# Kernel tuning notes

Hardware: AMD Instinct MI355X
Metric: run time of the kernel (lower is better)

## Reference

```python
import jax, jax.numpy as jnp
import numpy as np

D_MODEL = 1024
N_HEAD = 16
STRIDE = 16
HEAD_DIM = D_MODEL // N_HEAD
B, TQ, TK = 4, 2048, 8192
L = TK // STRIDE  # per-head key count (same for all heads since n_head <= stride and TK % stride == 0)


def setup_inputs() -> dict:
    key = jax.random.key(0)
    ks = jax.random.split(key, 12)
    w_scale = 0.02
    return {
        "q": jax.random.normal(ks[0], (B, TQ, D_MODEL), dtype=jnp.float32),
        "k": jax.random.normal(ks[1], (B, TK, D_MODEL), dtype=jnp.float32),
        "v": jax.random.normal(ks[2], (B, TK, D_MODEL), dtype=jnp.float32),
        "src_mask": jnp.ones((B, 1, 1, TK), dtype=jnp.int32),
        "w_q": jax.random.normal(ks[3], (D_MODEL, D_MODEL), dtype=jnp.float32) * w_scale,
        "b_q": jnp.zeros((D_MODEL,), dtype=jnp.float32),
        "w_k": jax.random.normal(ks[4], (D_MODEL, D_MODEL), dtype=jnp.float32) * w_scale,
        "b_k": jnp.zeros((D_MODEL,), dtype=jnp.float32),
        "w_v": jax.random.normal(ks[5], (D_MODEL, D_MODEL), dtype=jnp.float32) * w_scale,
        "b_v": jnp.zeros((D_MODEL,), dtype=jnp.float32),
        "w_o": jax.random.normal(ks[6], (D_MODEL, D_MODEL), dtype=jnp.float32) * w_scale,
        "b_o": jnp.zeros((D_MODEL,), dtype=jnp.float32),
    }


def reference(q, k, v, src_mask, w_q, b_q, w_k, b_k, w_v, b_v, w_o, b_o):
    # projections (torch Linear: x @ W.T + b)
    Q = (q @ w_q.T + b_q).reshape(B, TQ, N_HEAD, HEAD_DIM).transpose(0, 2, 1, 3)  # [B,H,Tq,D]
    K = (k @ w_k.T + b_k).reshape(B, TK, N_HEAD, HEAD_DIM).transpose(0, 2, 1, 3)  # [B,H,Tk,D]
    V = (v @ w_v.T + b_v).reshape(B, TK, N_HEAD, HEAD_DIM).transpose(0, 2, 1, 3)

    # HEPOS strided per-head key indices: head h attends to positions h, h+stride, ...
    idx = jnp.arange(N_HEAD)[:, None] + STRIDE * jnp.arange(L)[None, :]  # [H,L]
    gidx = idx[None, :, :, None]  # broadcastable over batch and head_dim
    Kh = jnp.take_along_axis(K, gidx, axis=2)  # [B,H,L,D]
    Vh = jnp.take_along_axis(V, gidx, axis=2)  # [B,H,L,D]

    scores = jnp.einsum("bhqd,bhld->bhql", Q, Kh) / jnp.sqrt(jnp.float32(HEAD_DIM))
    # gather per-head mask slice: src_mask [B,1,1,Tk] -> [B,H,1,L]
    mask_b = jnp.broadcast_to(src_mask, (B, N_HEAD, 1, TK))
    mask_h = jnp.take_along_axis(mask_b, idx[None, :, None, :], axis=3)  # [B,H,1,L]
    scores = jnp.where(mask_h == 0, jnp.float32(-1e9), scores)

    attn = jax.nn.softmax(scores, axis=-1)  # dropout is identity in eval mode
    out = jnp.einsum("bhql,bhld->bhqd", attn, Vh)  # [B,H,Tq,D]
    out = out.transpose(0, 2, 1, 3).reshape(B, TQ, D_MODEL)
    return out @ w_o.T + b_o
```

## Files before the change

### kernel.cpp

```cpp
#include <hip/hip_runtime.h>
#include <stdint.h>

#define NBATCH 4
#define TQ 2048
#define TKK 8192
#define DM 1024
#define HDIM 64
#define LLEN 512

typedef __bf16 bf16;
typedef __attribute__((ext_vector_type(4))) float f32x4;
typedef __attribute__((ext_vector_type(8))) __bf16 bf16x8;
typedef __attribute__((ext_vector_type(4))) __bf16 bf16x4;

typedef const __attribute__((address_space(1))) void* gas1_t;
typedef __attribute__((address_space(3))) void* las3_t;

__device__ __forceinline__ void gload_lds16(const void* g, void* l) {
  __builtin_amdgcn_global_load_lds((gas1_t)(uintptr_t)g, (las3_t)(uint32_t)(uintptr_t)l, 16, 0, 0);
}

__device__ __forceinline__ void cast4(const float* __restrict__ src, bf16* __restrict__ dst, int i) {
  float4 v = ((const float4*)src)[i];
  bf16x4 o;
  o[0] = (bf16)v.x; o[1] = (bf16)v.y; o[2] = (bf16)v.z; o[3] = (bf16)v.w;
  ((bf16x4*)dst)[i] = o;
}

__global__ void prep_kernel(const float* __restrict__ q,
                            const float* __restrict__ wq, const float* __restrict__ wk,
                            const float* __restrict__ wv, const float* __restrict__ wo,
                            const int* __restrict__ sm,
                            bf16* __restrict__ QB, bf16* __restrict__ WQ, bf16* __restrict__ WK,
                            bf16* __restrict__ WV, bf16* __restrict__ WO, float* __restrict__ MF) {
  int tid = blockIdx.x * blockDim.x + threadIdx.x;
  int stride = gridDim.x * blockDim.x;
  for (int i = tid; i < 2097152; i += stride) cast4(q, QB, i);
  for (int i = tid; i < 262144; i += stride) cast4(wq, WQ, i);
  for (int i = tid; i < 262144; i += stride) cast4(wk, WK, i);
  for (int i = tid; i < 262144; i += stride) cast4(wv, WV, i);
  for (int i = tid; i < 262144; i += stride) cast4(wo, WO, i);
  for (int i = tid; i < 32768; i += stride) {
    int bh = i >> 9, l = i & 511;
    int b = bh >> 4, h = bh & 15;
    MF[i] = sm[b * TKK + h + 16 * l] ? 1.0f : 0.0f;
  }
}

template<bool OUT_BF16>
__global__ __launch_bounds__(256) void gemm_bt_bias(
    const bf16* __restrict__ A, const bf16* __restrict__ Bm,
    const float* __restrict__ bias, void* __restrict__ Cout, float scale) {
  __shared__ bf16 As[128 * 64];
  __shared__ bf16 Bs[128 * 64];
  const int t = threadIdx.x;
  const int lane = t & 63, w = t >> 6;
  const int wm = w >> 1, wn = w & 1;
  const int bid = blockIdx.x;
  const int swz = (bid & 7) * 64 + (bid >> 3);
  const int m0 = (swz >> 3) * 128, n0 = (swz & 7) * 128;
  const int c = lane & 15, g = lane >> 4;
  f32x4 acc[4][4] = {};
  for (int k0 = 0; k0 < DM; k0 += 64) {
    __syncthreads();
    #pragma unroll
    for (int i = 0; i < 4; ++i) {
      int chunk = i * 256 + t;
      int row = chunk >> 3, blk = chunk & 7;
      gload_lds16(A + (size_t)(m0 + row) * DM + k0 + blk * 8, As + chunk * 8);
      gload_lds16(Bm + (size_t)(n0 + row) * DM + k0 + blk * 8, Bs + chunk * 8);
    }
    __syncthreads();
    #pragma unroll
    for (int kk = 0; kk < 2; ++kk) {
      bf16x8 af[4], bfr[4];
      #pragma unroll
      for (int f = 0; f < 4; ++f)
        af[f] = *(const bf16x8*)(As + (wm * 64 + f * 16 + c) * 64 + kk * 32 + g * 8);
      #pragma unroll
      for (int f = 0; f < 4; ++f)
        bfr[f] = *(const bf16x8*)(Bs + (wn * 64 + f * 16 + c) * 64 + kk * 32 + g * 8);
      #pragma unroll
      for (int mi = 0; mi < 4; ++mi)
        #pragma unroll
        for (int ni = 0; ni < 4; ++ni)
          acc[mi][ni] = __builtin_amdgcn_mfma_f32_16x16x32_bf16(af[mi], bfr[ni], acc[mi][ni], 0, 0, 0);
    }
  }
  #pragma unroll
  for (int ni = 0; ni < 4; ++ni) {
    int n = n0 + wn * 64 + ni * 16 + c;
    float bv = bias[n];
    #pragma unroll
    for (int mi = 0; mi < 4; ++mi) {
      int m = m0 + wm * 64 + mi * 16 + g * 4;
      #pragma unroll
      for (int j = 0; j < 4; ++j) {
        float vv = (acc[mi][ni][j] + bv) * scale;
        if (OUT_BF16) ((bf16*)Cout)[(size_t)(m + j) * DM + n] = (bf16)vv;
        else          ((float*)Cout)[(size_t)(m + j) * DM + n] = vv;
      }
    }
  }
}

__global__ __launch_bounds__(256) void kv_proj_fused(
    const float* __restrict__ Xk, const float* __restrict__ Xv,
    const bf16* __restrict__ WK, const bf16* __restrict__ WV,
    const float* __restrict__ bk, const float* __restrict__ bv,
    bf16* __restrict__ KH, bf16* __restrict__ VTT) {
  __shared__ bf16 As[64 * 64];
  __shared__ bf16 Bs[64 * 64];
  const int t = threadIdx.x, lane = t & 63, w = t >> 6;
  const int wm = w >> 1, wn = w & 1;
  const int bid = blockIdx.x;
  const int swz = (bid & 7) * 128 + (bid >> 3);
  const int iz = swz >> 9;
  const int bh = (swz >> 3) & 63;
  const int ltile = swz & 7;
  const int b = bh >> 4, h = bh & 15;
  const int l0 = ltile * 64;
  const float* __restrict__ X = iz ? Xv : Xk;
  const bf16* __restrict__ W = iz ? WV : WK;
  const float* __restrict__ bias = iz ? bv : bk;
  const int c = lane & 15, g = lane >> 4;
  f32x4 acc[2][2] = {};
  for (int k0 = 0; k0 < DM; k0 += 64) {
    __syncthreads();
    #pragma unroll
    for (int i = 0; i < 4; ++i) {
      int chunk = i * 256 + t;
      int row = chunk >> 4, q4 = chunk & 15;
      float4 vv = *(const float4*)(X + ((size_t)b * TKK + h + 16 * (l0 + row)) * DM + k0 + q4 * 4);
      bf16x4 o;
      o[0] = (bf16)vv.x; o[1] = (bf16)vv.y; o[2] = (bf16)vv.z; o[3] = (bf16)vv.w;
      uint32_t byte = (uint32_t)(row * 128 + q4 * 8) ^ (uint32_t)((row & 7) << 4);
      *(bf16x4*)((char*)As + byte) = o;
    }
    #pragma unroll
    for (int i = 0; i < 2; ++i) {
      int chunk = i * 256 + t;
      int row = chunk >> 3, blk = chunk & 7;
      uint4 vv = *(const uint4*)(W + (size_t)(h * 64 + row) * DM + k0 + blk * 8);
      uint32_t byte = (uint32_t)(row * 128 + blk * 16) ^ (uint32_t)((row & 7) << 4);
      *(uint4*)((char*)Bs + byte) = vv;
    }
    __syncthreads();
    #pragma unroll
    for (int kk = 0; kk < 2; ++kk) {
      bf16x8 af[2], bfr[2];
      #pragma unroll
      for (int f = 0; f < 2; ++f) {
        int row = wm * 32 + f * 16 + c;
        uint32_t byte = (uint32_t)(row * 128 + (kk * 32 + g * 8) * 2) ^ (uint32_t)((row & 7) << 4);
        af[f] = *(const bf16x8*)((char*)As + byte);
      }
      #pragma unroll
      for (int f = 0; f < 2; ++f) {
        int row = wn * 32 + f * 16 + c;
        uint32_t byte = (uint32_t)(row * 128 + (kk * 32 + g * 8) * 2) ^ (uint32_t)((row & 7) << 4);
        bfr[f] = *(const bf16x8*)((char*)Bs + byte);
      }
      #pragma unroll
      for (int mi = 0; mi < 2; ++mi)
        #pragma unroll
        for (int ni = 0; ni < 2; ++ni)
          acc[mi][ni] = __builtin_amdgcn_mfma_f32_16x16x32_bf16(af[mi], bfr[ni], acc[mi][ni], 0, 0, 0);
    }
  }
  #pragma unroll
  for (int ni = 0; ni < 2; ++ni) {
    int n = wn * 32 + ni * 16 + c;
    float bvv = bias[h * 64 + n];
    #pragma unroll
    for (int mi = 0; mi < 2; ++mi) {
      int m = wm * 32 + mi * 16 + g * 4;
      if (iz == 0) {
        #pragma unroll
        for (int j = 0; j < 4; ++j)
          KH[((size_t)bh * LLEN + l0 + m + j) * 64 + n] = (bf16)(acc[mi][ni][j] + bvv);
      } else {
        bf16x4 o;
        #pragma unroll
        for (int j = 0; j < 4; ++j) o[j] = (bf16)(acc[mi][ni][j] + bvv);
        *(bf16x4*)(VTT + ((size_t)bh * 64 + n) * LLEN + l0 + m) = o;
      }
    }
  }
}

__device__ __forceinline__ void stage_kv(const bf16* __restrict__ KH, const bf16* __restrict__ VT,
                                         bf16* Ks, bf16* Vs, int bh, int lt, int t) {
  #pragma unroll
  for (int i = 0; i < 4; ++i) {
    int chunk = i * 256 + t, row = chunk >> 3, blk = chunk & 7;
    uint4 v = *(const uint4*)(KH + ((size_t)bh * LLEN + lt * 128 + row) * 64 + blk * 8);
    uint32_t byte = (uint32_t)(row * 128 + blk * 16) ^ (uint32_t)((row & 7) << 4);
    *(uint4*)((char*)Ks + byte) = v;
  }
  #pragma unroll
  for (int i = 0; i < 4; ++i) {
    int chunk = i * 256 + t, row = chunk >> 4, blk = chunk & 15;
    uint4 v = *(const uint4*)(VT + ((size_t)bh * 64 + row) * LLEN + lt * 128 + blk * 8);
    uint32_t byte = (uint32_t)(row * 256 + blk * 16) ^ (uint32_t)((row & 7) << 4);
    *(uint4*)((char*)Vs + byte) = v;
  }
}

__global__ __launch_bounds__(256) void attn_kernel(
    const bf16* __restrict__ Qp, const bf16* __restrict__ KH, const bf16* __restrict__ VT,
    const float* __restrict__ maskf, bf16* __restrict__ AO) {
  __shared__ bf16 Qs[128 * 64];
  __shared__ bf16 Ks[128 * 64];
  __shared__ bf16 Vs[64 * 128];
  const int t = threadIdx.x, lane = t & 63, w = t >> 6;
  const int bid = blockIdx.x;
  const int swz = (bid & 7) * 128 + (bid >> 3);
  const int bh = swz >> 4, b = bh >> 4, h = bh & 15;
  const int q0 = (swz & 15) * 128;
  const int c = lane & 15, g = lane >> 4;

  #pragma unroll
  for (int i = 0; i < 4; ++i) {
    int chunk = i * 256 + t, row = chunk >> 3, blk = chunk & 7;
    uint4 v = *(const uint4*)(Qp + ((size_t)(b * TQ + q0 + row)) * DM + h * 64 + blk * 8);
    uint32_t byte = (uint32_t)(row * 128 + blk * 16) ^ (uint32_t)((row & 7) << 4);
    *(uint4*)((char*)Qs + byte) = v;
  }
  stage_kv(KH, VT, Ks, Vs, bh, 0, t);
  __syncthreads();

  bf16x8 bq[2][2];
  #pragma unroll
  for (int nf = 0; nf < 2; ++nf)
    #pragma unroll
    for (int kk = 0; kk < 2; ++kk) {
      int row = w * 32 + nf * 16 + c;
      uint32_t byte = (uint32_t)(row * 128 + (kk * 32 + g * 8) * 2) ^ (uint32_t)((row & 7) << 4);
      bq[nf][kk] = *(const bf16x8*)((char*)Qs + byte);
    }

  float m_run[2] = {-1e30f, -1e30f};
  float l_run[2] = {0.0f, 0.0f};
  f32x4 acc_o[4][2] = {};

  #pragma unroll 1
  for (int lt = 0; lt < 4; ++lt) {
    f32x4 s[8][2] = {};
    #pragma unroll
    for (int kk = 0; kk < 2; ++kk) {
      bf16x8 ak[8];
      #pragma unroll
      for (int mf = 0; mf < 8; ++mf) {
        int row = mf * 16 + c;
        uint32_t byte = (uint32_t)(row * 128 + (kk * 32 + g * 8) * 2) ^ (uint32_t)((row & 7) << 4);
        ak[mf] = *(const bf16x8*)((char*)Ks + byte);
      }
      __builtin_amdgcn_s_setprio(1);
      #pragma unroll
      for (int mf = 0; mf < 8; ++mf)
        #pragma unroll
        for (int nf = 0; nf < 2; ++nf)
          s[mf][nf] = __builtin_amdgcn_mfma_f32_16x16x32_bf16(ak[mf], bq[nf][kk], s[mf][nf], 0, 0, 0);
      __builtin_amdgcn_s_setprio(0);
    }
    #pragma unroll
    for (int nf = 0; nf < 2; ++nf) {
      float mnew = m_run[nf];
      #pragma unroll
      for (int mf = 0; mf < 8; ++mf)
        #pragma unroll
        for (int j = 0; j < 4; ++j)
          mnew = fmaxf(mnew, s[mf][nf][j]);
      mnew = fmaxf(mnew, __shfl_xor(mnew, 16));
      mnew = fmaxf(mnew, __shfl_xor(mnew, 32));
      float fs = exp2f((m_run[nf] - mnew) * 1.44269504f);
      m_run[nf] = mnew;
      float rs = 0.0f;
      #pragma unroll
      for (int mf = 0; mf < 8; ++mf) {
        float4 mk = *(const float4*)(maskf + (size_t)bh * LLEN + lt * 128 + mf * 16 + 4 * g);
        #pragma unroll
        for (int j = 0; j < 4; ++j) {
          float p = exp2f((s[mf][nf][j] - mnew) * 1.44269504f) * ((const float*)&mk)[j];
          s[mf][nf][j] = p;
          rs += p;
        }
      }
      rs += __shfl_xor(rs, 16);
      rs += __shfl_xor(rs, 32);
      l_run[nf] = l_run[nf] * fs + rs;
      #pragma unroll
      for (int mf = 0; mf < 4; ++mf) acc_o[mf][nf] *= fs;
    }
    #pragma unroll
    for (int kk = 0; kk < 4; ++kk) {
      bf16x8 pb[2];
      #pragma unroll
      for (int nf = 0; nf < 2; ++nf)
        #pragma unroll
        for (int s8 = 0; s8 < 8; ++s8)
          pb[nf][s8] = (bf16)s[kk * 2 + (s8 >> 2)][nf][s8 & 3];
      #pragma unroll
      for (int mf = 0; mf < 4; ++mf) {
        int d = mf * 16 + c;
        uint32_t base = (uint32_t)(d * 256 + (kk * 32 + g * 4) * 2);
        uint32_t swzb = (uint32_t)((d & 7) << 4);
        bf16x4 lo = *(const bf16x4*)((char*)Vs + (base ^ swzb));
        bf16x4 hi = *(const bf16x4*)((char*)Vs + ((base + 32) ^ swzb));
        bf16x8 av = __builtin_shufflevector(lo, hi, 0, 1, 2, 3, 4, 5, 6, 7);
        __builtin_amdgcn_s_setprio(1);
        #pragma unroll
        for (int nf = 0; nf < 2; ++nf)
          acc_o[mf][nf] = __builtin_amdgcn_mfma_f32_16x16x32_bf16(av, pb[nf], acc_o[mf][nf], 0, 0, 0);
        __builtin_amdgcn_s_setprio(0);
      }
    }
    if (lt < 3) {
      __syncthreads();
      stage_kv(KH, VT, Ks, Vs, bh, lt + 1, t);
      __syncthreads();
    }
  }
  #pragma unroll
  for (int nf = 0; nf < 2; ++nf) {
    float inv = 1.0f / l_run[nf];
    int qq = q0 + w * 32 + nf * 16 + c;
    #pragma unroll
    for (int mf = 0; mf < 4; ++mf) {
      bf16x4 o;
      #pragma unroll
      for (int j = 0; j < 4; ++j) o[j] = (bf16)(acc_o[mf][nf][j] * inv);
      *(bf16x4*)(AO + ((size_t)(b * TQ + qq)) * DM + h * 64 + mf * 16 + 4 * g) = o;
    }
  }
}

extern "C" void kernel_launch(void* const* d_in, const int* in_sizes, int n_in,
                              void* d_out, int out_size, void* d_ws, size_t ws_size,
                              hipStream_t stream) {
  const float* q   = (const float*)d_in[0];
  const float* k   = (const float*)d_in[1];
  const float* v   = (const float*)d_in[2];
  const int*  smk  = (const int*)d_in[3];
  const float* w_q = (const float*)d_in[4];
  const float* b_q = (const float*)d_in[5];
  const float* w_k = (const float*)d_in[6];
  const float* b_k = (const float*)d_in[7];
  const float* w_v = (const float*)d_in[8];
  const float* b_v = (const float*)d_in[9];
  const float* w_o = (const float*)d_in[10];
  const float* b_o = (const float*)d_in[11];
  float* out = (float*)d_out;

  bf16* WS  = (bf16*)d_ws;
  bf16* WQ  = WS;
  bf16* WK  = WQ + (1u << 20);
  bf16* WV  = WK + (1u << 20);
  bf16* WO  = WV + (1u << 20);
  bf16* QB  = WO + (1u << 20);
  bf16* QP  = QB + (8u << 20);
  bf16* KH  = QP + (8u << 20);
  bf16* VTT = KH + (2u << 20);
  bf16* AO  = VTT + (2u << 20);
  float* MF = (float*)(AO + (8u << 20));

  prep_kernel<<<2048, 256, 0, stream>>>(q, w_q, w_k, w_v, w_o, smk, QB, WQ, WK, WV, WO, MF);
  gemm_bt_bias<true><<<512, 256, 0, stream>>>(QB, WQ, b_q, QP, 0.125f);
  kv_proj_fused<<<1024, 256, 0, stream>>>(k, v, WK, WV, b_k, b_v, KH, VTT);
  attn_kernel<<<1024, 256, 0, stream>>>(QP, KH, VTT, MF, AO);
  gemm_bt_bias<false><<<512, 256, 0, stream>>>(AO, WO, b_o, out, 1.0f);
}
```

Baseline: 504.9 us.

## Restructure K/V projection into 16-row full-K tiles with weights read directly

Replaces the 64x64-tile K-loop GEMM for the strided K/V projection with a kernel where each block loads 16 gathered input rows across the full 1024-wide reduction into LDS once. Each wave then streams its 16 weight rows straight from global memory into MFMA fragments, with no weight staging and only one barrier. The grid grows from 1024 to 4096 blocks. This removes the per-K-step syncs and smaller staging, but weights are re-read per block from global/L2 and each block does little MFMA work.

```diff
diff --git a/kernel.cpp b/kernel.cpp
--- a/kernel.cpp
+++ b/kernel.cpp
@@ -104,88 +104,55 @@
   }
 }
 
-__global__ __launch_bounds__(256) void kv_proj_fused(
+__global__ __launch_bounds__(256) void kv_proj2(
     const float* __restrict__ Xk, const float* __restrict__ Xv,
     const bf16* __restrict__ WK, const bf16* __restrict__ WV,
     const float* __restrict__ bk, const float* __restrict__ bv,
     bf16* __restrict__ KH, bf16* __restrict__ VTT) {
-  __shared__ bf16 As[64 * 64];
-  __shared__ bf16 Bs[64 * 64];
+  __shared__ bf16 As[16 * 1024];
   const int t = threadIdx.x, lane = t & 63, w = t >> 6;
-  const int wm = w >> 1, wn = w & 1;
   const int bid = blockIdx.x;
-  const int swz = (bid & 7) * 128 + (bid >> 3);
-  const int iz = swz >> 9;
-  const int bh = (swz >> 3) & 63;
-  const int ltile = swz & 7;
+  const int swz = (bid & 7) * 512 + (bid >> 3);
+  const int iz = swz >> 11;
+  const int bh = (swz >> 5) & 63;
+  const int l0 = (swz & 31) * 16;
   const int b = bh >> 4, h = bh & 15;
-  const int l0 = ltile * 64;
   const float* __restrict__ X = iz ? Xv : Xk;
   const bf16* __restrict__ W = iz ? WV : WK;
   const float* __restrict__ bias = iz ? bv : bk;
   const int c = lane & 15, g = lane >> 4;
-  f32x4 acc[2][2] = {};
-  for (int k0 = 0; k0 < DM; k0 += 64) {
-    __syncthreads();
-    #pragma unroll
-    for (int i = 0; i < 4; ++i) {
-      int chunk = i * 256 + t;
-      int row = chunk >> 4, q4 = chunk & 15;
-      float4 vv = *(const float4*)(X + ((size_t)b * TKK + h + 16 * (l0 + row)) * DM + k0 + q4 * 4);
-      bf16x4 o;
-      o[0] = (bf16)vv.x; o[1] = (bf16)vv.y; o[2] = (bf16)vv.z; o[3] = (bf16)vv.w;
-      uint32_t byte = (uint32_t)(row * 128 + q4 * 8) ^ (uint32_t)((row & 7) << 4);
-      *(bf16x4*)((char*)As + byte) = o;
-    }
-    #pragma unroll
-    for (int i = 0; i < 2; ++i) {
-      int chunk = i * 256 + t;
-      int row = chunk >> 3, blk = chunk & 7;
-      uint4 vv = *(const uint4*)(W + (size_t)(h * 64 + row) * DM + k0 + blk * 8);
-      uint32_t byte = (uint32_t)(row * 128 + blk * 16) ^ (uint32_t)((row & 7) << 4);
-      *(uint4*)((char*)Bs + byte) = vv;
-    }
-    __syncthreads();
-    #pragma unroll
-    for (int kk = 0; kk < 2; ++kk) {
-      bf16x8 af[2], bfr[2];
-      #pragma unroll
-      for (int f = 0; f < 2; ++f) {
-        int row = wm * 32 + f * 16 + c;
-        uint32_t byte = (uint32_t)(row * 128 + (kk * 32 + g * 8) * 2) ^ (uint32_t)((row & 7) << 4);
-        af[f] = *(const bf16x8*)((char*)As + byte);
-      }
-      #pragma unroll
-      for (int f = 0; f < 2; ++f) {
-        int row = wn * 32 + f * 16 + c;
-        uint32_t byte = (uint32_t)(row * 128 + (kk * 32 + g * 8) * 2) ^ (uint32_t)((row & 7) << 4);
-        bfr[f] = *(const bf16x8*)((char*)Bs + byte);
-      }
-      #pragma unroll
-      for (int mi = 0; mi < 2; ++mi)
-        #pragma unroll
-        for (int ni = 0; ni < 2; ++ni)
-          acc[mi][ni] = __builtin_amdgcn_mfma_f32_16x16x32_bf16(af[mi], bfr[ni], acc[mi][ni], 0, 0, 0);
-    }
-  }
-  #pragma unroll
-  for (int ni = 0; ni < 2; ++ni) {
-    int n = wn * 32 + ni * 16 + c;
-    float bvv = bias[h * 64 + n];
-    #pragma unroll
-    for (int mi = 0; mi < 2; ++mi) {
-      int m = wm * 32 + mi * 16 + g * 4;
-      if (iz == 0) {
-        #pragma unroll
-        for (int j = 0; j < 4; ++j)
-          KH[((size_t)bh * LLEN + l0 + m + j) * 64 + n] = (bf16)(acc[mi][ni][j] + bvv);
-      } else {
-        bf16x4 o;
-        #pragma unroll
-        for (int j = 0; j < 4; ++j) o[j] = (bf16)(acc[mi][ni][j] + bvv);
-        *(bf16x4*)(VTT + ((size_t)bh * 64 + n) * LLEN + l0 + m) = o;
-      }
-    }
+
+  #pragma unroll
+  for (int r = 0; r < 16; ++r) {
+    float4 vv = *(const float4*)(X + ((size_t)b * TKK + h + 16 * (l0 + r)) * DM + t * 4);
+    bf16x4 o;
+    o[0] = (bf16)vv.x; o[1] = (bf16)vv.y; o[2] = (bf16)vv.z; o[3] = (bf16)vv.w;
+    uint32_t byte = (uint32_t)(r * 2048 + t * 8) ^ (uint32_t)((r & 7) << 4);
+    *(bf16x4*)((char*)As + byte) = o;
+  }
+  __syncthreads();
+
+  const bf16* __restrict__ Wb = W + (size_t)(h * 64 + w * 16 + c) * DM;
+  f32x4 acc = {};
+  #pragma unroll
+  for (int ks = 0; ks < 32; ++ks) {
+    int k0 = ks * 32;
+    uint32_t byte = (uint32_t)(c * 2048 + (k0 + g * 8) * 2) ^ (uint32_t)((c & 7) << 4);
+    bf16x8 a = *(const bf16x8*)((char*)As + byte);
+    bf16x8 bfrag = *(const bf16x8*)(Wb + k0 + g * 8);
+    acc = __builtin_amdgcn_mfma_f32_16x16x32_bf16(a, bfrag, acc, 0, 0, 0);
+  }
+  const int d = w * 16 + c;
+  const float bvv = bias[h * 64 + d];
+  if (iz == 0) {
+    #pragma unroll
+    for (int j = 0; j < 4; ++j)
+      KH[((size_t)bh * LLEN + l0 + 4 * g + j) * 64 + d] = (bf16)(acc[j] + bvv);
+  } else {
+    bf16x4 o;
+    #pragma unroll
+    for (int j = 0; j < 4; ++j) o[j] = (bf16)(acc[j] + bvv);
+    *(bf16x4*)(VTT + ((size_t)bh * 64 + d) * LLEN + l0 + 4 * g) = o;
   }
 }
 
@@ -367,7 +334,7 @@
 
   prep_kernel<<<2048, 256, 0, stream>>>(q, w_q, w_k, w_v, w_o, smk, QB, WQ, WK, WV, WO, MF);
   gemm_bt_bias<true><<<512, 256, 0, stream>>>(QB, WQ, b_q, QP, 0.125f);
-  kv_proj_fused<<<1024, 256, 0, stream>>>(k, v, WK, WV, b_k, b_v, KH, VTT);
+  kv_proj2<<<4096, 256, 0, stream>>>(k, v, WK, WV, b_k, b_v, KH, VTT);
   attn_kernel<<<1024, 256, 0, stream>>>(QP, KH, VTT, MF, AO);
   gemm_bt_bias<false><<<512, 256, 0, stream>>>(AO, WO, b_o, out, 1.0f);
 }
```

Measured after the change: 498.5 us. Within noise of the previous version (-1.3%).
